# Kernel optimization log

Hardware: AMD Instinct MI355X
Metric: run time of the kernel (lower is better)

The kernel has to match this reference:

```python
import jax, jax.numpy as jnp
import numpy as np

B, K = 16, 50
IN_CH, N_CLASSES, N_ANCH = 256, 80, 3
STRIDE, FSIZE, IGNORE_THRE = 8, 76, 0.7
N_CH = 5 + N_CLASSES
ANCHORS = np.array([[10,13],[16,30],[33,23],[30,61],[62,45],[59,119],[116,90],[156,198],[373,326]], np.float32)
ALL_GRID = ANCHORS / STRIDE            # all 9 anchors in grid units
ANCH_MASK = np.array([0, 1, 2])        # layer_no = 2
MASKED = ALL_GRID[ANCH_MASK]           # (3,2) anchors used by this head


def setup_inputs():
    key = jax.random.key(0)
    k1, k2, k3, k4, k5, k6 = jax.random.split(key, 6)
    xin = jax.random.normal(k1, (B, IN_CH, FSIZE, FSIZE), jnp.float32)
    cls = jax.random.randint(k2, (B, K), 0, N_CLASSES).astype(jnp.float32)
    xy = jax.random.uniform(k3, (B, K, 2), minval=0.05, maxval=0.95)
    wh = jax.random.uniform(k4, (B, K, 2), minval=0.02, maxval=0.30)
    labels = jnp.concatenate([cls[..., None], xy, wh], -1)   # (B,K,5) [cls,xc,yc,w,h]
    oc = N_ANCH * N_CH
    conv_w = jax.random.normal(k5, (oc, IN_CH), jnp.float32) * 0.01
    conv_b = jax.random.normal(k6, (oc,), jnp.float32) * 0.01
    return {"xin": xin, "labels": labels, "conv_w": conv_w, "conv_b": conv_b}


def _yolo(xin, conv_w, conv_b, labels):
    f, C = FSIZE, N_CLASSES
    # 1x1 conv == channel matmul
    raw = jnp.einsum('bchw,oc->bohw', xin, conv_w) + conv_b[None, :, None, None]
    raw = raw.reshape(B, N_ANCH, N_CH, f, f).transpose(0, 1, 3, 4, 2)  # (B,A,f,f,85)
    # sigmoid on x,y,obj,cls; w,h stay raw
    out = jnp.concatenate([jax.nn.sigmoid(raw[..., :2]), raw[..., 2:4], jax.nn.sigmoid(raw[..., 4:])], -1)

    grid = jnp.arange(f, dtype=jnp.float32)
    mw = jnp.asarray(MASKED[:, 0]); mh = jnp.asarray(MASKED[:, 1])
    px = out[..., 0] + grid[None, None, None, :]
    py = out[..., 1] + grid[None, None, :, None]
    pw = jnp.exp(out[..., 2]) * mw[None, :, None, None]
    ph = jnp.exp(out[..., 3]) * mh[None, :, None, None]
    pred = jax.lax.stop_gradient(jnp.stack([px, py, pw, ph], -1))  # detached, like torch .data

    labels = jax.lax.stop_gradient(labels)
    valid = labels.sum(-1) > 0                  # (B,K) padding rows are all-zero
    tx = labels[..., 1] * f; ty = labels[..., 2] * f
    tw = labels[..., 3] * f; th = labels[..., 4] * f
    ii = tx.astype(jnp.int32); jj = ty.astype(jnp.int32)

    # anchor matching: IoU of [0,0,w,h] truth vs [0,0,aw,ah] ref anchors (corners at origin)
    aw = jnp.asarray(ALL_GRID[:, 0]); ah = jnp.asarray(ALL_GRID[:, 1])
    inter_a = jnp.minimum(tw[..., None], aw) * jnp.minimum(th[..., None], ah)  # (B,K,9)
    iou_a = inter_a / (tw[..., None] * th[..., None] + aw * ah - inter_a)
    best_n_all = jnp.argmax(iou_a, -1)
    best_n = best_n_all % 3
    best_mask = (best_n_all == ANCH_MASK[0]) | (best_n_all == ANCH_MASK[1]) | (best_n_all == ANCH_MASK[2])

    # pred-vs-truth IoU in cxcywh form (xyxy=False)
    pa = pred.reshape(B, -1, 4)                 # (B, A*f*f, 4)
    tb = jnp.stack([tx, ty, tw, th], -1)        # (B, K, 4)
    tl = jnp.maximum(pa[:, :, None, :2] - pa[:, :, None, 2:] * 0.5, tb[:, None, :, :2] - tb[:, None, :, 2:] * 0.5)
    br = jnp.minimum(pa[:, :, None, :2] + pa[:, :, None, 2:] * 0.5, tb[:, None, :, :2] + tb[:, None, :, 2:] * 0.5)
    en = jnp.all(tl < br, -1)
    inter = jnp.prod(br - tl, -1) * en
    area_p = pa[..., 2] * pa[..., 3]; area_t = tb[..., 2] * tb[..., 3]
    iou_p = inter / (area_p[:, :, None] + area_t[:, None, :] - inter)
    iou_p = jnp.where(valid[:, None, :], iou_p, 0.0)
    ignore = (iou_p.max(-1) > IGNORE_THRE).reshape(B, N_ANCH, f, f)
    obj_mask = 1.0 - ignore.astype(jnp.float32)

    # scatter positive targets; non-selected rows routed out-of-bounds and dropped
    sel = valid & best_mask
    bb = jnp.where(sel, jnp.arange(B)[:, None], B)
    obj_mask = obj_mask.at[bb, best_n, jj, ii].set(1.0, mode='drop')
    tgt_mask = jnp.zeros((B, N_ANCH, f, f, 4 + C)).at[bb, best_n, jj, ii].set(1.0, mode='drop')
    scale = jnp.sqrt(2.0 - tw * th / (f * f))
    tgt_scale = jnp.zeros((B, N_ANCH, f, f, 2)).at[bb, best_n, jj, ii].set(
        jnp.broadcast_to(scale[..., None], (B, K, 2)), mode='drop')
    tvals = jnp.concatenate([
        (tx - ii)[..., None], (ty - jj)[..., None],
        jnp.log(tw / mw[best_n] + 1e-16)[..., None],
        jnp.log(th / mh[best_n] + 1e-16)[..., None],
        jnp.ones((B, K, 1), jnp.float32),
        jax.nn.one_hot(labels[..., 0].astype(jnp.int32), C)], -1)  # (B,K,85)
    target = jnp.zeros((B, N_ANCH, f, f, N_CH)).at[bb, best_n, jj, ii].set(tvals, mode='drop')

    oxy = out[..., :2] * tgt_mask[..., :2]
    owh = out[..., 2:4] * tgt_mask[..., 2:4] * tgt_scale
    oob = out[..., 4] * obj_mask
    ocl = out[..., 5:] * tgt_mask[..., 4:]
    txy = target[..., :2] * tgt_mask[..., :2]
    twh = target[..., 2:4] * tgt_mask[..., 2:4] * tgt_scale
    tob = target[..., 4] * obj_mask
    tcl = target[..., 5:] * tgt_mask[..., 4:]

    def bce(p, t, w=None):
        pc = jnp.clip(p, 1e-12, 1.0 - 1e-7)
        e = -(t * jnp.log(pc) + (1.0 - t) * jnp.log(1.0 - pc))
        if w is not None:
            e = e * w
        return e.sum()

    loss_xy = bce(oxy, txy, tgt_scale * tgt_scale)
    loss_wh = 0.5 * jnp.sum((owh - twh) ** 2)
    loss_obj = bce(oob, tob)
    loss_cls = bce(ocl, tcl)
    out_m = jnp.concatenate([oxy, owh, oob[..., None], ocl], -1)
    tgt_m = jnp.concatenate([txy, twh, tob[..., None], tcl], -1)
    loss_l2 = jnp.sum((out_m - tgt_m) ** 2)
    loss = loss_xy + loss_wh + loss_obj + loss_cls
    return loss, loss_xy, loss_wh, loss_obj, loss_cls, loss_l2, out_m


def reference(xin, labels, conv_w, conv_b):
    return _yolo(xin, conv_w, conv_b, labels)
```

## Files before the change

kernel.cpp:

```cpp
#include <hip/hip_runtime.h>
#include <hip/hip_bf16.h>

#define B_   16
#define K_   50
#define CIN  256
#define F_   76
#define A_   3
#define NCH  85
#define OC   255
#define HW   (F_*F_)
#define NBLK (B_*F_)
#define NCELL (A_*F_)

#define WS_BIAS_F 32768
#define WS_LAB_F  33024
#define WS_PART_F 45824

typedef __attribute__((ext_vector_type(8))) short short8;
typedef __attribute__((ext_vector_type(4))) float f32x4;

__device__ __constant__ float AW9[9] = {1.25f, 2.0f, 4.125f, 3.75f, 7.75f, 7.375f, 14.5f, 19.5f, 46.625f};
__device__ __constant__ float AH9[9] = {1.625f, 3.75f, 2.875f, 7.625f, 5.625f, 14.875f, 11.25f, 24.75f, 40.75f};

__device__ __forceinline__ unsigned short f2bf(float f) {
    union { float f; unsigned int u; } v; v.f = f;
    unsigned int r = v.u + 0x7fffu + ((v.u >> 16) & 1u);
    return (unsigned short)(r >> 16);
}
__device__ __forceinline__ float bf2f(unsigned short b) {
    union { unsigned int u; float f; } v; v.u = ((unsigned int)b) << 16;
    return v.f;
}
__device__ __forceinline__ float sigm(float r) { return 1.0f / (1.0f + __expf(-r)); }
__device__ __forceinline__ float bce_t(float p, float tv) {
    float pc = fminf(fmaxf(p, 1e-12f), 1.0f - 1e-7f);
    return -(tv * __logf(pc) + (1.0f - tv) * __logf(1.0f - pc));
}

__global__ void prep_kernel(const float* __restrict__ conv_w, const float* __restrict__ conv_b,
                            const float* __restrict__ labels, float* __restrict__ ws) {
    int bid = blockIdx.x, t = threadIdx.x;
    if (bid < 256) {
        int idx = bid * 256 + t;
        int mt = idx >> 12, ks = (idx >> 9) & 7, lane = (idx >> 3) & 63, jj = idx & 7;
        int row = mt * 16 + (lane & 15);
        int k   = ks * 32 + (lane >> 4) * 8 + jj;
        float v = (row < OC) ? conv_w[row * CIN + k] : 0.0f;
        ((unsigned short*)ws)[idx] = f2bf(v);
    } else if (bid == 256) {
        ws[WS_BIAS_F + t] = (t < OC) ? conv_b[t] : 0.0f;
    } else {
        for (int idx = t; idx < B_ * K_; idx += 256) {
            const float* L = labels + idx * 5;
            float cls = L[0], xc = L[1], yc = L[2], wl = L[3], hl = L[4];
            float ssum = cls + xc + yc + wl + hl;
            float validf = (ssum > 0.0f) ? 1.0f : 0.0f;
            float tx = xc * F_, ty = yc * F_, tw = wl * F_, th = hl * F_;
            int ii = (int)tx, jj = (int)ty;
            float tarea = tw * th;
            float best = -1.0f; int bn = 0;
            #pragma unroll
            for (int n = 0; n < 9; n++) {
                float inter = fminf(tw, AW9[n]) * fminf(th, AH9[n]);
                float iou = inter / (tarea + AW9[n] * AH9[n] - inter);
                if (iou > best) { best = iou; bn = n; }
            }
            int a = bn % 3;
            bool self = (validf != 0.0f) && (bn < 3);
            float* R = ws + WS_LAB_F + idx * 16;
            R[0] = tx; R[1] = ty; R[2] = tw; R[3] = th;
            R[4] = validf; R[5] = self ? (float)a : -1.0f; R[6] = (float)ii; R[7] = (float)jj;
            R[8] = tx - (float)ii; R[9] = ty - (float)jj;
            R[10] = __logf(tw / AW9[a] + 1e-16f);
            R[11] = __logf(th / AH9[a] + 1e-16f);
            R[12] = sqrtf(2.0f - tarea / (float)HW);
            R[13] = cls; R[14] = 0.0f; R[15] = 0.0f;
        }
    }
}

__global__ __launch_bounds__(512, 4) void yolo_main(const float* __restrict__ xin,
                                                    const float* __restrict__ ws,
                                                    float* __restrict__ d_out,
                                                    float* __restrict__ part) {
    __shared__ __align__(16) unsigned short UNI[19456];
    __shared__ float4 LAB[K_ * 4];
    __shared__ float biasS[256];
    __shared__ int   flagS[NCELL];
    __shared__ float omvS[NCELL];
    __shared__ float redS[8][5];

    const int t = threadIdx.x;
    const int b = blockIdx.x / F_;
    const int j = blockIdx.x % F_;

    if (t < 256) biasS[t] = ws[WS_BIAS_F + t];
    if (t < K_ * 4) LAB[t] = ((const float4*)(ws + WS_LAB_F + b * (K_ * 16)))[t];

    for (int idx = t; idx < 32 * F_; idx += 512) {
        int co = idx / F_, i = idx - co * F_;
        const float* xp = xin + ((size_t)b * CIN + co * 8) * HW + j * F_ + i;
        short8 v;
        #pragma unroll
        for (int jj = 0; jj < 8; jj++) v[jj] = (short)f2bf(xp[jj * HW]);
        int phys = co ^ (i & 7);
        *(short8*)&UNI[i * 256 + phys * 8] = v;
    }
    __syncthreads();

    const int w = t >> 6, lane = t & 63, lr = lane & 15, q = lane >> 4;
    f32x4 acc[2][5];
    #pragma unroll
    for (int m = 0; m < 2; m++)
        #pragma unroll
        for (int n = 0; n < 5; n++) acc[m][n] = (f32x4){0.0f, 0.0f, 0.0f, 0.0f};

    const short8* wf = (const short8*)ws;
    #pragma unroll 2
    for (int ks = 0; ks < 8; ks++) {
        short8 afr[2], bfr[5];
        #pragma unroll
        for (int m = 0; m < 2; m++)
            afr[m] = wf[((w + m * 8) * 8 + ks) * 64 + lane];
        #pragma unroll
        for (int n = 0; n < 5; n++) {
            int nn = n * 16 + lr;
            int phys = (ks * 4 + q) ^ (nn & 7);
            bfr[n] = *(const short8*)&UNI[nn * 256 + phys * 8];
        }
        #pragma unroll
        for (int m = 0; m < 2; m++)
            #pragma unroll
            for (int n = 0; n < 5; n++)
                acc[m][n] = __builtin_amdgcn_mfma_f32_16x16x32_bf16(afr[m], bfr[n], acc[m][n], 0, 0, 0);
    }
    __syncthreads();

    #pragma unroll
    for (int m = 0; m < 2; m++) {
        #pragma unroll
        for (int n = 0; n < 5; n++) {
            int i = n * 16 + lr;
            if (i < F_) {
                #pragma unroll
                for (int r = 0; r < 4; r++) {
                    int o = (w + m * 8) * 16 + q * 4 + r;
                    if (o < OC) {
                        int a  = o / NCH;
                        int ch = o - a * NCH;
                        UNI[(a * F_ + i) * NCH + ch] = f2bf(acc[m][n][r] + biasS[o]);
                    }
                }
            }
        }
    }
    __syncthreads();

    float lxy = 0.0f, lwh = 0.0f, lobj = 0.0f, lcls = 0.0f, l2 = 0.0f;
    if (t < NCELL) {
        int a = t / F_, i = t - a * F_;
        const unsigned short* rc = UNI + t * NCH;
        float x   = sigm(bf2f(rc[0]));
        float y   = sigm(bf2f(rc[1]));
        float wr  = bf2f(rc[2]);
        float hr  = bf2f(rc[3]);
        float obj = sigm(bf2f(rc[4]));

        float px = x + (float)i, py = y + (float)j;
        float pw = __expf(wr) * AW9[a], ph = __expf(hr) * AH9[a];
        float hpw = pw * 0.5f, hph = ph * 0.5f;
        float areap = pw * ph;
        float fa_t = (float)a, fi_t = (float)i, fj_t = (float)j;

        float maxiou = 0.0f; int mk = -1;
        #pragma unroll 2
        for (int k = 0; k < K_; k++) {
            float4 A0 = LAB[4 * k + 0];
            float4 A1 = LAB[4 * k + 1];
            float tx = A0.x, ty = A0.y, tw = A0.z, th = A0.w;
            float tlx = fmaxf(px - hpw, tx - tw * 0.5f);
            float tly = fmaxf(py - hph, ty - th * 0.5f);
            float brx = fminf(px + hpw, tx + tw * 0.5f);
            float bry = fminf(py + hph, ty + th * 0.5f);
            float iw = brx - tlx, ih = bry - tly;
            float inter = (iw > 0.0f && ih > 0.0f) ? iw * ih : 0.0f;
            float iou = __fdividef(inter, areap + tw * th - inter);
            iou = (A1.x != 0.0f) ? iou : 0.0f;
            maxiou = fmaxf(maxiou, iou);
            bool match = (A1.y == fa_t) & (A1.z == fi_t) & (A1.w == fj_t);
            mk = match ? k : mk;
        }
        float objmask = (maxiou > 0.7f) ? 0.0f : 1.0f;

        if (mk >= 0) {
            float4 B0 = LAB[4 * mk + 2];
            float4 B1 = LAB[4 * mk + 3];
            float sc = B1.x, sc2 = sc * sc;
            float txv = B0.x, tyv = B0.y, twv = B0.z, thv = B0.w;
            int cl = (int)B1.y;
            lxy = (bce_t(x, txv) + bce_t(y, tyv)) * sc2;
            float dw = wr - twv, dh = hr - thv;
            lwh = 0.5f * sc2 * (dw * dw + dh * dh);
            float pco = fminf(fmaxf(obj, 1e-12f), 1.0f - 1e-7f);
            lobj = -__logf(pco);
            float dx = x - txv, dy = y - tyv, dob = obj - 1.0f;
            l2 = dx * dx + dy * dy + sc2 * (dw * dw + dh * dh) + dob * dob;
            for (int c = 0; c < 80; c++) {
                float p = sigm(bf2f(rc[5 + c]));
                float tcv = (c == cl) ? 1.0f : 0.0f;
                lcls += bce_t(p, tcv);
                float d = p - tcv;
                l2 += d * d;
            }
            flagS[t] = mk + 1;
            omvS[t]  = obj;
        } else {
            float oo = obj * objmask;
            if (objmask != 0.0f) {
                float pco = fminf(obj, 1.0f - 1e-7f);
                lobj = -__logf(1.0f - pco);
            }
            l2 = oo * oo;
            flagS[t] = 0;
            omvS[t]  = oo;
        }
    }
    __syncthreads();

    for (int a = 0; a < A_; a++) {
        float2* dst = (float2*)(d_out + 6 + (size_t)((b * A_ + a) * F_ + j) * F_ * NCH);
        for (int idx2 = t; idx2 < (F_ * NCH) / 2; idx2 += 512) {
            int p = idx2 << 1;
            int i0 = p / NCH;
            int c0 = p - i0 * NCH;
            int i1 = i0, c1 = c0 + 1;
            if (c1 == NCH) { i1++; c1 = 0; }
            float v[2];
            int iv[2] = {i0, i1}, cv[2] = {c0, c1};
            #pragma unroll
            for (int e = 0; e < 2; e++) {
                int cell = a * F_ + iv[e];
                int flag = flagS[cell];
                if (flag == 0) {
                    v[e] = (cv[e] == 4) ? omvS[cell] : 0.0f;
                } else {
                    float raw = bf2f(UNI[cell * NCH + cv[e]]);
                    if (cv[e] == 2 || cv[e] == 3) v[e] = raw * LAB[4 * (flag - 1) + 3].x;
                    else                          v[e] = sigm(raw);
                }
            }
            dst[idx2] = make_float2(v[0], v[1]);
        }
    }

    #pragma unroll
    for (int off = 32; off > 0; off >>= 1) {
        lxy  += __shfl_down(lxy, off);
        lwh  += __shfl_down(lwh, off);
        lobj += __shfl_down(lobj, off);
        lcls += __shfl_down(lcls, off);
        l2   += __shfl_down(l2, off);
    }
    if (lane == 0) {
        redS[w][0] = lxy; redS[w][1] = lwh; redS[w][2] = lobj;
        redS[w][3] = lcls; redS[w][4] = l2;
    }
    __syncthreads();
    if (t == 0) {
        float* P = part + (size_t)blockIdx.x * 8;
        #pragma unroll
        for (int q2 = 0; q2 < 5; q2++) {
            float s = 0.0f;
            #pragma unroll
            for (int ww = 0; ww < 8; ww++) s += redS[ww][q2];
            P[q2] = s;
        }
    }
}

__global__ void finish_kernel(const float* __restrict__ part, float* __restrict__ d_out) {
    int t = threadIdx.x;
    float s0 = 0, s1 = 0, s2 = 0, s3 = 0, s4 = 0;
    for (int bidx = t; bidx < NBLK; bidx += 256) {
        const float* P = part + (size_t)bidx * 8;
        s0 += P[0]; s1 += P[1]; s2 += P[2]; s3 += P[3]; s4 += P[4];
    }
    #pragma unroll
    for (int off = 32; off > 0; off >>= 1) {
        s0 += __shfl_down(s0, off); s1 += __shfl_down(s1, off);
        s2 += __shfl_down(s2, off); s3 += __shfl_down(s3, off);
        s4 += __shfl_down(s4, off);
    }
    __shared__ float red[4][5];
    if ((t & 63) == 0) {
        int w = t >> 6;
        red[w][0] = s0; red[w][1] = s1; red[w][2] = s2; red[w][3] = s3; red[w][4] = s4;
    }
    __syncthreads();
    if (t == 0) {
        float r0 = red[0][0] + red[1][0] + red[2][0] + red[3][0];
        float r1 = red[0][1] + red[1][1] + red[2][1] + red[3][1];
        float r2 = red[0][2] + red[1][2] + red[2][2] + red[3][2];
        float r3 = red[0][3] + red[1][3] + red[2][3] + red[3][3];
        float r4 = red[0][4] + red[1][4] + red[2][4] + red[3][4];
        d_out[0] = r0 + r1 + r2 + r3;
        d_out[1] = r0; d_out[2] = r1; d_out[3] = r2; d_out[4] = r3; d_out[5] = r4;
    }
}

extern "C" void kernel_launch(void* const* d_in, const int* in_sizes, int n_in,
                              void* d_out, int out_size, void* d_ws, size_t ws_size,
                              hipStream_t stream) {
    const float* xin    = (const float*)d_in[0];
    const float* labels = (const float*)d_in[1];
    const float* conv_w = (const float*)d_in[2];
    const float* conv_b = (const float*)d_in[3];
    float* out  = (float*)d_out;
    float* ws   = (float*)d_ws;
    float* part = ws + WS_PART_F;

    prep_kernel<<<258, 256, 0, stream>>>(conv_w, conv_b, labels, ws);
    yolo_main<<<NBLK, 512, 0, stream>>>(xin, ws, out, part);
    finish_kernel<<<1, 256, 0, stream>>>(part, out);
}
```

Baseline: 234.7 us.

## Compute only box/objectness channels densely; evaluate class logits only at matched cells

The full 255-channel 1x1 conv is replaced by a small MFMA kernel that computes only the 15 x/y/w/h/obj channels per cell and stages them in the output buffer. A finalize kernel then writes the masked output. For each matched target cell it recomputes the 80 class logits with a scalar dot product over the input column. This removes the dense class-channel matmul, which is needed only at the few matched cells because the masked output is zero elsewhere. The cost is an extra launch, a global round-trip of the staged raw values, and serialized per-target work with block-wide syncs.

```diff
diff --git a/kernel.cpp b/kernel.cpp
--- a/kernel.cpp
+++ b/kernel.cpp
@@ -11,10 +11,12 @@
 #define HW   (F_*F_)
 #define NBLK (B_*F_)
 #define NCELL (A_*F_)
+#define SLAB (F_*NCH)
 
 #define WS_BIAS_F 32768
 #define WS_LAB_F  33024
 #define WS_PART_F 45824
+#define WS_W15_F  55552
 
 typedef __attribute__((ext_vector_type(8))) short short8;
 typedef __attribute__((ext_vector_type(4))) float f32x4;
@@ -41,15 +43,11 @@
                             const float* __restrict__ labels, float* __restrict__ ws) {
     int bid = blockIdx.x, t = threadIdx.x;
     if (bid < 256) {
-        int idx = bid * 256 + t;
-        int mt = idx >> 12, ks = (idx >> 9) & 7, lane = (idx >> 3) & 63, jj = idx & 7;
-        int row = mt * 16 + (lane & 15);
-        int k   = ks * 32 + (lane >> 4) * 8 + jj;
-        float v = (row < OC) ? conv_w[row * CIN + k] : 0.0f;
-        ((unsigned short*)ws)[idx] = f2bf(v);
+        float v = (t < OC) ? conv_w[t * CIN + bid] : 0.0f;
+        ((unsigned short*)ws)[bid * 256 + t] = f2bf(v);
     } else if (bid == 256) {
         ws[WS_BIAS_F + t] = (t < OC) ? conv_b[t] : 0.0f;
-    } else {
+    } else if (bid == 257) {
         for (int idx = t; idx < B_ * K_; idx += 256) {
             const float* L = labels + idx * 5;
             float cls = L[0], xc = L[1], yc = L[2], wl = L[3], hl = L[4];
@@ -76,95 +74,91 @@
             R[12] = sqrtf(2.0f - tarea / (float)HW);
             R[13] = cls; R[14] = 0.0f; R[15] = 0.0f;
         }
-    }
-}
-
-__global__ __launch_bounds__(512, 4) void yolo_main(const float* __restrict__ xin,
+    } else {
+        unsigned short* wf = (unsigned short*)(ws + WS_W15_F);
+        for (int idx = t; idx < 4096; idx += 256) {
+            int ks = idx >> 9, lane = (idx >> 3) & 63, jj = idx & 7;
+            int row = lane & 15;
+            int k = ks * 32 + (lane >> 4) * 8 + jj;
+            float v = 0.0f;
+            if (row < 15) v = conv_w[((row / 5) * NCH + (row % 5)) * CIN + k];
+            wf[idx] = f2bf(v);
+        }
+    }
+}
+
+__global__ __launch_bounds__(256) void conv5_kernel(const float* __restrict__ xin,
                                                     const float* __restrict__ ws,
-                                                    float* __restrict__ d_out,
-                                                    float* __restrict__ part) {
-    __shared__ __align__(16) unsigned short UNI[19456];
+                                                    float* __restrict__ d_out) {
+    const int w = threadIdx.x >> 6, lane = threadIdx.x & 63;
+    const int lr = lane & 15, q = lane >> 4;
+    const int T = blockIdx.x * 4 + w;
+    const int b = T / 361;
+    const int col0 = (T - b * 361) * 16;
+
+    const unsigned short* wf15 = (const unsigned short*)(ws + WS_W15_F);
+    short8 afr[8];
+    #pragma unroll
+    for (int ks = 0; ks < 8; ks++)
+        afr[ks] = *(const short8*)&wf15[(ks * 64 + lane) * 8];
+
+    f32x4 acc = (f32x4){0.0f, 0.0f, 0.0f, 0.0f};
+    const float* xbase = xin + (size_t)b * CIN * HW + col0 + lr;
+    #pragma unroll
+    for (int ks = 0; ks < 8; ks++) {
+        int kb = ks * 32 + q * 8;
+        float xv[8];
+        #pragma unroll
+        for (int jj = 0; jj < 8; jj++) xv[jj] = xbase[(size_t)(kb + jj) * HW];
+        union { short8 s; __hip_bfloat162 h[4]; } u;
+        #pragma unroll
+        for (int p = 0; p < 4; p++)
+            u.h[p] = __float22bfloat162_rn(make_float2(xv[2 * p], xv[2 * p + 1]));
+        acc = __builtin_amdgcn_mfma_f32_16x16x32_bf16(afr[ks], u.s, acc, 0, 0, 0);
+    }
+
+    const int pos = col0 + lr;
+    const int j = pos / F_, i = pos - j * F_;
+    float* slab0 = d_out + 6 + (size_t)((b * A_) * F_ + j) * SLAB;
+    const float* biasg = ws + WS_BIAS_F;
+    #pragma unroll
+    for (int r = 0; r < 4; r++) {
+        int row = q * 4 + r;
+        if (row < 15) {
+            int o = (row / 5) * NCH + (row % 5);
+            slab0[row * F_ + i] = acc[r] + biasg[o];
+        }
+    }
+}
+
+__global__ __launch_bounds__(256) void finalize_kernel(const float* __restrict__ xin,
+                                                       const float* __restrict__ ws,
+                                                       float* __restrict__ d_out,
+                                                       float* __restrict__ part) {
+    __shared__ float raw5S[15 * F_];
     __shared__ float4 LAB[K_ * 4];
-    __shared__ float biasS[256];
     __shared__ int   flagS[NCELL];
     __shared__ float omvS[NCELL];
-    __shared__ float redS[8][5];
+    __shared__ float xcolS[256];
+    __shared__ float redS[4][5];
 
     const int t = threadIdx.x;
     const int b = blockIdx.x / F_;
     const int j = blockIdx.x % F_;
 
-    if (t < 256) biasS[t] = ws[WS_BIAS_F + t];
+    const float* rawg = d_out + 6 + (size_t)((b * A_) * F_ + j) * SLAB;
+    for (int idx = t; idx < 15 * F_; idx += 256) raw5S[idx] = rawg[idx];
     if (t < K_ * 4) LAB[t] = ((const float4*)(ws + WS_LAB_F + b * (K_ * 16)))[t];
-
-    for (int idx = t; idx < 32 * F_; idx += 512) {
-        int co = idx / F_, i = idx - co * F_;
-        const float* xp = xin + ((size_t)b * CIN + co * 8) * HW + j * F_ + i;
-        short8 v;
-        #pragma unroll
-        for (int jj = 0; jj < 8; jj++) v[jj] = (short)f2bf(xp[jj * HW]);
-        int phys = co ^ (i & 7);
-        *(short8*)&UNI[i * 256 + phys * 8] = v;
-    }
-    __syncthreads();
-
-    const int w = t >> 6, lane = t & 63, lr = lane & 15, q = lane >> 4;
-    f32x4 acc[2][5];
-    #pragma unroll
-    for (int m = 0; m < 2; m++)
-        #pragma unroll
-        for (int n = 0; n < 5; n++) acc[m][n] = (f32x4){0.0f, 0.0f, 0.0f, 0.0f};
-
-    const short8* wf = (const short8*)ws;
-    #pragma unroll 2
-    for (int ks = 0; ks < 8; ks++) {
-        short8 afr[2], bfr[5];
-        #pragma unroll
-        for (int m = 0; m < 2; m++)
-            afr[m] = wf[((w + m * 8) * 8 + ks) * 64 + lane];
-        #pragma unroll
-        for (int n = 0; n < 5; n++) {
-            int nn = n * 16 + lr;
-            int phys = (ks * 4 + q) ^ (nn & 7);
-            bfr[n] = *(const short8*)&UNI[nn * 256 + phys * 8];
-        }
-        #pragma unroll
-        for (int m = 0; m < 2; m++)
-            #pragma unroll
-            for (int n = 0; n < 5; n++)
-                acc[m][n] = __builtin_amdgcn_mfma_f32_16x16x32_bf16(afr[m], bfr[n], acc[m][n], 0, 0, 0);
-    }
-    __syncthreads();
-
-    #pragma unroll
-    for (int m = 0; m < 2; m++) {
-        #pragma unroll
-        for (int n = 0; n < 5; n++) {
-            int i = n * 16 + lr;
-            if (i < F_) {
-                #pragma unroll
-                for (int r = 0; r < 4; r++) {
-                    int o = (w + m * 8) * 16 + q * 4 + r;
-                    if (o < OC) {
-                        int a  = o / NCH;
-                        int ch = o - a * NCH;
-                        UNI[(a * F_ + i) * NCH + ch] = f2bf(acc[m][n][r] + biasS[o]);
-                    }
-                }
-            }
-        }
-    }
     __syncthreads();
 
     float lxy = 0.0f, lwh = 0.0f, lobj = 0.0f, lcls = 0.0f, l2 = 0.0f;
     if (t < NCELL) {
         int a = t / F_, i = t - a * F_;
-        const unsigned short* rc = UNI + t * NCH;
-        float x   = sigm(bf2f(rc[0]));
-        float y   = sigm(bf2f(rc[1]));
-        float wr  = bf2f(rc[2]);
-        float hr  = bf2f(rc[3]);
-        float obj = sigm(bf2f(rc[4]));
+        float x   = sigm(raw5S[(a * 5 + 0) * F_ + i]);
+        float y   = sigm(raw5S[(a * 5 + 1) * F_ + i]);
+        float wr  = raw5S[(a * 5 + 2) * F_ + i];
+        float hr  = raw5S[(a * 5 + 3) * F_ + i];
+        float obj = sigm(raw5S[(a * 5 + 4) * F_ + i]);
 
         float px = x + (float)i, py = y + (float)j;
         float pw = __expf(wr) * AW9[a], ph = __expf(hr) * AH9[a];
@@ -197,7 +191,6 @@
             float4 B1 = LAB[4 * mk + 3];
             float sc = B1.x, sc2 = sc * sc;
             float txv = B0.x, tyv = B0.y, twv = B0.z, thv = B0.w;
-            int cl = (int)B1.y;
             lxy = (bce_t(x, txv) + bce_t(y, tyv)) * sc2;
             float dw = wr - twv, dh = hr - thv;
             lwh = 0.5f * sc2 * (dw * dw + dh * dh);
@@ -205,13 +198,6 @@
             lobj = -__logf(pco);
             float dx = x - txv, dy = y - tyv, dob = obj - 1.0f;
             l2 = dx * dx + dy * dy + sc2 * (dw * dw + dh * dh) + dob * dob;
-            for (int c = 0; c < 80; c++) {
-                float p = sigm(bf2f(rc[5 + c]));
-                float tcv = (c == cl) ? 1.0f : 0.0f;
-                lcls += bce_t(p, tcv);
-                float d = p - tcv;
-                l2 += d * d;
-            }
             flagS[t] = mk + 1;
             omvS[t]  = obj;
         } else {
@@ -228,31 +214,61 @@
     __syncthreads();
 
     for (int a = 0; a < A_; a++) {
-        float2* dst = (float2*)(d_out + 6 + (size_t)((b * A_ + a) * F_ + j) * F_ * NCH);
-        for (int idx2 = t; idx2 < (F_ * NCH) / 2; idx2 += 512) {
+        float2* dst = (float2*)(d_out + 6 + (size_t)((b * A_ + a) * F_ + j) * SLAB);
+        for (int idx2 = t; idx2 < SLAB / 2; idx2 += 256) {
             int p = idx2 << 1;
-            int i0 = p / NCH;
-            int c0 = p - i0 * NCH;
+            int i0 = p / NCH, c0 = p - i0 * NCH;
             int i1 = i0, c1 = c0 + 1;
             if (c1 == NCH) { i1++; c1 = 0; }
-            float v[2];
-            int iv[2] = {i0, i1}, cv[2] = {c0, c1};
-            #pragma unroll
-            for (int e = 0; e < 2; e++) {
-                int cell = a * F_ + iv[e];
-                int flag = flagS[cell];
-                if (flag == 0) {
-                    v[e] = (cv[e] == 4) ? omvS[cell] : 0.0f;
-                } else {
-                    float raw = bf2f(UNI[cell * NCH + cv[e]]);
-                    if (cv[e] == 2 || cv[e] == 3) v[e] = raw * LAB[4 * (flag - 1) + 3].x;
-                    else                          v[e] = sigm(raw);
-                }
+            float v0 = (c0 == 4) ? omvS[a * F_ + i0] : 0.0f;
+            float v1 = (c1 == 4) ? omvS[a * F_ + i1] : 0.0f;
+            dst[idx2] = make_float2(v0, v1);
+        }
+    }
+    __threadfence_block();
+    __syncthreads();
+
+    const unsigned short* Wtg = (const unsigned short*)ws;
+    const float* biasg = ws + WS_BIAS_F;
+    for (int k = 0; k < K_; k++) {
+        float4 A1 = LAB[4 * k + 1];
+        int fa = (int)A1.y;
+        if (fa < 0) continue;
+        if ((int)A1.w != j) continue;
+        int fi = (int)A1.z;
+        int cell = fa * F_ + fi;
+        if (flagS[cell] != k + 1) continue;
+
+        xcolS[t] = xin[((size_t)b * CIN + t) * HW + j * F_ + fi];
+        __syncthreads();
+        float4 B1 = LAB[4 * k + 3];
+        float sc = B1.x; int cl = (int)B1.y;
+        if (t < NCH) {
+            float v; int chout;
+            if (t < 80) {
+                int o = fa * NCH + 5 + t;
+                float accv = biasg[o];
+                #pragma unroll 8
+                for (int kk = 0; kk < 256; kk++)
+                    accv += bf2f(Wtg[kk * 256 + o]) * xcolS[kk];
+                float p = sigm(accv);
+                float tcv = (t == cl) ? 1.0f : 0.0f;
+                lcls += bce_t(p, tcv);
+                float d = p - tcv;
+                l2 += d * d;
+                v = p; chout = 5 + t;
+            } else {
+                int ch = t - 80;
+                float raw = raw5S[(fa * 5 + ch) * F_ + fi];
+                v = (ch == 2 || ch == 3) ? raw * sc : sigm(raw);
+                chout = ch;
             }
-            dst[idx2] = make_float2(v[0], v[1]);
-        }
-    }
-
+            d_out[6 + (size_t)((b * A_ + fa) * F_ + j) * SLAB + fi * NCH + chout] = v;
+        }
+        __syncthreads();
+    }
+
+    const int w = t >> 6, lane = t & 63;
     #pragma unroll
     for (int off = 32; off > 0; off >>= 1) {
         lxy  += __shfl_down(lxy, off);
@@ -269,12 +285,8 @@
     if (t == 0) {
         float* P = part + (size_t)blockIdx.x * 8;
         #pragma unroll
-        for (int q2 = 0; q2 < 5; q2++) {
-            float s = 0.0f;
-            #pragma unroll
-            for (int ww = 0; ww < 8; ww++) s += redS[ww][q2];
-            P[q2] = s;
-        }
+        for (int q2 = 0; q2 < 5; q2++)
+            P[q2] = redS[0][q2] + redS[1][q2] + redS[2][q2] + redS[3][q2];
     }
 }
 
@@ -319,7 +331,8 @@
     float* ws   = (float*)d_ws;
     float* part = ws + WS_PART_F;
 
-    prep_kernel<<<258, 256, 0, stream>>>(conv_w, conv_b, labels, ws);
-    yolo_main<<<NBLK, 512, 0, stream>>>(xin, ws, out, part);
+    prep_kernel<<<259, 256, 0, stream>>>(conv_w, conv_b, labels, ws);
+    conv5_kernel<<<5776 / 4, 256, 0, stream>>>(xin, ws, out);
+    finalize_kernel<<<NBLK, 256, 0, stream>>>(xin, ws, out, part);
     finish_kernel<<<1, 256, 0, stream>>>(part, out);
 }
```

Measured after the change: 213.7 us. 1.1x faster.
